# Optimization experiments

Hardware: AMD Instinct MI355X
Metric: run time of the kernel (lower is better)

Reference implementation:

```python
import jax, jax.numpy as jnp
import numpy as np

B = 4096
P_HID = 1024
H_HID = 512
MAX_P = 128
MAX_HE = MAX_P // 3  # 42
TAU = 1.0
EPS = 1e-20


def setup_inputs() -> dict:
    key = jax.random.key(0)
    ks = jax.random.split(key, 12)
    s_p = 1.0 / np.sqrt(P_HID)
    s_h = 1.0 / np.sqrt(H_HID)
    # gumbel noise: g = -log(-log(U))
    u_p = jax.random.uniform(ks[3], (B, MAX_P, 2), minval=EPS, maxval=1.0)
    u_h = jax.random.uniform(ks[4], (B, MAX_HE, 2), minval=EPS, maxval=1.0)
    return {
        "particle_h": jax.random.normal(ks[0], (B, P_HID), jnp.float32),
        "edge_h": jax.random.normal(ks[1], (B, H_HID), jnp.float32),
        "hyperedge_h": jax.random.normal(ks[2], (B, H_HID), jnp.float32),
        "g_p": -jnp.log(-jnp.log(u_p)),
        "g_h": -jnp.log(-jnp.log(u_h)),
        "W1_p": jax.random.normal(ks[5], (P_HID, P_HID), jnp.float32) * s_p,
        "b1_p": jnp.zeros((P_HID,), jnp.float32),
        "W2_p": jax.random.normal(ks[6], (P_HID, MAX_P), jnp.float32) * s_p,
        "b2_p": jnp.zeros((MAX_P,), jnp.float32),
        "W1_h": jax.random.normal(ks[7], (H_HID, H_HID), jnp.float32) * s_h,
        "b1_h": jnp.zeros((H_HID,), jnp.float32),
        "W2_h": jax.random.normal(ks[8], (H_HID, MAX_HE), jnp.float32) * s_h,
        "b2_h": jnp.zeros((MAX_HE,), jnp.float32),
    }


def _gumbel_hard_st(logits, g, tau):
    """F.gumbel_softmax(stack([l,-l],-1), tau, hard=True)[...,0] (straight-through)."""
    y = jax.nn.softmax((jnp.stack([logits, -logits], axis=-1) + g) / tau, axis=-1)
    y0 = y[..., 0]
    hard0 = (y0 > y[..., 1]).astype(y0.dtype)
    return hard0 + y0 - jax.lax.stop_gradient(y0)


def _mlp(x, W1, b1, W2, b2):
    return jax.nn.gelu(x @ W1 + b1, approximate=False) @ W2 + b2


def reference(particle_h, edge_h, hyperedge_h, g_p, g_h,
              W1_p, b1_p, W2_p, b2_p, W1_h, b1_h, W2_h, b2_h):
    particle_logits = _mlp(particle_h, W1_p, b1_p, W2_p, b2_p)      # [B, MAX_P]
    particle_mask = _gumbel_hard_st(particle_logits, g_p, TAU)      # [B, MAX_P]
    n_particles = particle_mask.sum(axis=-1).astype(jnp.int32)      # [B]

    # Ragged edge lists as a fixed padded buffer: all C(MAX_P,2) lexicographic
    # pairs (same order as torch.combinations); pair (i,j), i<j, is valid for
    # batch b iff j < n_particles[b].
    ii, jj = jnp.triu_indices(MAX_P, k=1)
    edge_index = jnp.stack([ii, jj]).astype(jnp.int32)              # [2, E_max]
    edge_valid = jj[None, :] < n_particles[:, None]                 # [B, E_max] bool

    hyperedge_logits = _mlp(hyperedge_h, W1_h, b1_h, W2_h, b2_h)    # [B, MAX_HE]
    hyperedge_mask = _gumbel_hard_st(hyperedge_logits, g_h, TAU)
    n_hyperedges = hyperedge_mask.sum(axis=-1).astype(jnp.int32)

    return (particle_mask, n_particles, edge_index, edge_valid,
            hyperedge_mask, n_hyperedges)
```

## Files before the change

### kernel.cpp

```cpp
#include <hip/hip_runtime.h>
#include <hip/hip_bf16.h>
#include <math.h>

typedef __bf16 bf16_t;
typedef bf16_t bf16x8 __attribute__((ext_vector_type(8)));
typedef bf16_t bf16x4 __attribute__((ext_vector_type(4)));
typedef float f32x4 __attribute__((ext_vector_type(4)));
typedef int i32x4 __attribute__((ext_vector_type(4)));
typedef unsigned int u32;

#define B_SZ 4096
#define P_HID 1024
#define H_HID 512
#define MAX_P 128
#define MAX_HE 42
#define HE_PAD 128
#define E_MAX 8128
#define E_MAX4 2032

__device__ __forceinline__ void async_cp16(const bf16_t* g, bf16_t* l) {
    __builtin_amdgcn_global_load_lds(
        (const __attribute__((address_space(1))) u32*)g,
        (__attribute__((address_space(3))) u32*)l, 16, 0, 0);
}

__device__ __forceinline__ float gelu_exact(float v) {
    return 0.5f * v * (1.f + erff(v * 0.70710678118654752f));
}

struct GemmP {
    const bf16_t *Ahi, *Alo, *BThi, *BTlo;
    const float* bias;
    bf16_t *Chi, *Clo;
    const float* g;
    float *out_mask, *out_n;
    int *ws_n;
    int N, K, NV, nx;
};

template<int MODE, int BM>
__global__ __launch_bounds__(256, 3) void gemm_pack(GemmP P, GemmP H, int pBlocks)
{
    constexpr int BN = 128;
    constexpr int MT = BM / 32;
    constexpr int NT = 4;
    constexpr int OPS_A = BM / 16;
    constexpr int OPS_B = BN / 16;
    constexpr int NOPS = 2 * OPS_A + 2 * OPS_B;
    constexpr int TILE = NOPS * 16 * 32;

    __shared__ __align__(16) bf16_t smem[2 * TILE];
    __shared__ float cnt[BM][2];

    const bool isP = (int)blockIdx.x < pBlocks;
    const GemmP& a = isP ? P : H;
    const int bid  = isP ? blockIdx.x : blockIdx.x - pBlocks;
    const int bn   = (bid % a.nx) * BN;
    const int bm   = (bid / a.nx) * BM;
    const int K    = a.K;

    const int tid  = threadIdx.x;
    const int lane = tid & 63;
    const int wid  = tid >> 6;
    const int wm   = wid & 1;
    const int wn   = wid >> 1;

    const int srow = lane >> 2;
    const int scol = (lane & 3) * 8;
    const int fr   = lane & 15;
    const int fq   = lane >> 4;

    f32x4 acc[MT][NT];
#pragma unroll
    for (int i = 0; i < MT; ++i)
#pragma unroll
        for (int j = 0; j < NT; ++j)
            acc[i][j] = (f32x4){0.f, 0.f, 0.f, 0.f};

    const bf16_t* const gA0 = a.Ahi  + (size_t)bm * K;
    const bf16_t* const gA1 = a.Alo  + (size_t)bm * K;
    const bf16_t* const gB0 = a.BThi + (size_t)bn * K;
    const bf16_t* const gB1 = a.BTlo + (size_t)bn * K;

    auto stage = [&](int buf, int kt) {
#pragma unroll
        for (int o = 0; o < NOPS; ++o) {
            if ((o & 3) != wid) continue;
            const bf16_t* gsrc;
            int q, sec;
            if (o < OPS_A)                  { q = o;                     gsrc = gA0; sec = 0; }
            else if (o < 2 * OPS_A)         { q = o - OPS_A;             gsrc = gA1; sec = BM * 32; }
            else if (o < 2 * OPS_A + OPS_B) { q = o - 2 * OPS_A;         gsrc = gB0; sec = 2 * BM * 32; }
            else                            { q = o - 2 * OPS_A - OPS_B; gsrc = gB1; sec = 2 * BM * 32 + BN * 32; }
            async_cp16(gsrc + (size_t)(q * 16 + srow) * K + kt + scol,
                       smem + buf * TILE + sec + q * 16 * 32);
        }
    };

    stage(0, 0);
    __syncthreads();
    int cur = 0;
    for (int kt = 0; kt < K; kt += 32) {
        if (kt + 32 < K) stage(cur ^ 1, kt + 32);

        const bf16_t* const Tb = smem + cur * TILE;
        bf16x8 ah[MT], al[MT];
#pragma unroll
        for (int i = 0; i < MT; ++i) {
            const int row = wm * (BM / 2) + i * 16 + fr;
            ah[i] = *(const bf16x8*)(Tb + row * 32 + fq * 8);
            al[i] = *(const bf16x8*)(Tb + BM * 32 + row * 32 + fq * 8);
        }
#pragma unroll
        for (int j = 0; j < NT; ++j) {
            const int row = wn * 64 + j * 16 + fr;
            const bf16x8 bh = *(const bf16x8*)(Tb + 2 * BM * 32 + row * 32 + fq * 8);
            const bf16x8 bl = *(const bf16x8*)(Tb + 2 * BM * 32 + BN * 32 + row * 32 + fq * 8);
#pragma unroll
            for (int i = 0; i < MT; ++i) {
                acc[i][j] = __builtin_amdgcn_mfma_f32_16x16x32_bf16(ah[i], bh, acc[i][j], 0, 0, 0);
                acc[i][j] = __builtin_amdgcn_mfma_f32_16x16x32_bf16(ah[i], bl, acc[i][j], 0, 0, 0);
                acc[i][j] = __builtin_amdgcn_mfma_f32_16x16x32_bf16(al[i], bh, acc[i][j], 0, 0, 0);
            }
        }
        __syncthreads();
        cur ^= 1;
    }

    if (MODE == 0) {
#pragma unroll
        for (int i = 0; i < MT; ++i)
#pragma unroll
            for (int j = 0; j < NT; ++j) {
                const int col  = bn + wn * 64 + j * 16 + fr;
                const int row0 = bm + wm * (BM / 2) + i * 16 + fq * 4;
                const float bj = a.bias[col];
#pragma unroll
                for (int r = 0; r < 4; ++r) {
                    float v = gelu_exact(acc[i][j][r] + bj);
                    bf16_t h = (bf16_t)v;
                    bf16_t l = (bf16_t)(v - (float)h);
                    const size_t off = (size_t)(row0 + r) * a.N + col;
                    a.Chi[off] = h;
                    a.Clo[off] = l;
                }
            }
    } else {
        const int NV = a.NV;
#pragma unroll
        for (int i = 0; i < MT; ++i) {
#pragma unroll
            for (int r = 0; r < 4; ++r) {
                const int row_l = wm * (BM / 2) + i * 16 + fq * 4 + r;
                const int grow  = bm + row_l;
                float s = 0.f;
#pragma unroll
                for (int j = 0; j < NT; ++j) {
                    const int col = wn * 64 + j * 16 + fr;
                    if (col < NV) {
                        const float v = acc[i][j][r] + a.bias[col];
                        const size_t idx = (size_t)grow * NV + col;
                        const float g0 = a.g[2 * idx + 0];
                        const float g1 = a.g[2 * idx + 1];
                        const float m = ((v + g0) > (g1 - v)) ? 1.f : 0.f;
                        a.out_mask[idx] = m;
                        s += m;
                    }
                }
                s += __shfl_xor(s, 1, 64);
                s += __shfl_xor(s, 2, 64);
                s += __shfl_xor(s, 4, 64);
                s += __shfl_xor(s, 8, 64);
                if (fr == 0) cnt[row_l][wn] = s;
            }
        }
        __syncthreads();
        if (tid < BM) {
            const float c = cnt[tid][0] + cnt[tid][1];
            a.out_n[bm + tid] = c;
            if (a.ws_n) a.ws_n[bm + tid] = (int)c;
        }
    }
}

struct PrepArgs {
    const float *ph, *hh, *W1p, *W2p, *W1h, *W2h;
    bf16_t *pA_hi, *pA_lo, *hA_hi, *hA_lo;
    bf16_t *W1pT_hi, *W1pT_lo, *W2pT_hi, *W2pT_lo;
    bf16_t *W1hT_hi, *W1hT_lo, *W2hT_hi, *W2hT_lo;
    float *out_ei; int *ws_jj;
};

__device__ __forceinline__ void split4(const float* x, bf16_t* hi, bf16_t* lo, int i) {
    float4 v = ((const float4*)x)[i];
    float vv[4] = {v.x, v.y, v.z, v.w};
    bf16x4 h, l;
#pragma unroll
    for (int r = 0; r < 4; ++r) {
        bf16_t hh = (bf16_t)vv[r];
        h[r] = hh;
        l[r] = (bf16_t)(vv[r] - (float)hh);
    }
    ((bf16x4*)hi)[i] = h;
    ((bf16x4*)lo)[i] = l;
}

__device__ __forceinline__ void tsplit(
    const float* W, bf16_t* Thi, bf16_t* Tlo, int K, int N,
    int t, int nx, float (*sh)[33], int tid)
{
    const int n0 = (t % nx) * 32, k0 = (t / nx) * 32;
    const int tx = tid & 31, ty = tid >> 5;
    for (int r = ty; r < 32; r += 8) {
        const int n = n0 + tx;
        sh[r][tx] = (n < N) ? W[(size_t)(k0 + r) * N + n] : 0.f;
    }
    __syncthreads();
    for (int r = ty; r < 32; r += 8) {
        const float x = sh[tx][r];
        bf16_t h = (bf16_t)x;
        bf16_t l = (bf16_t)(x - (float)h);
        const size_t off = (size_t)(n0 + r) * K + k0 + tx;
        Thi[off] = h;
        Tlo[off] = l;
    }
}

__device__ __forceinline__ int tri_off(int i) { return (i * (255 - i)) >> 1; }

__global__ __launch_bounds__(256) void prep_all(PrepArgs a)
{
    __shared__ float sh[32][33];
    const int bid = blockIdx.x;
    const int tid = threadIdx.x;

    if (bid < 4096) {
        split4(a.ph, a.pA_hi, a.pA_lo, bid * 256 + tid);
    } else if (bid < 6144) {
        split4(a.hh, a.hA_hi, a.hA_lo, (bid - 4096) * 256 + tid);
    } else if (bid < 7168) {
        tsplit(a.W1p, a.W1pT_hi, a.W1pT_lo, P_HID, P_HID, bid - 6144, 32, sh, tid);
    } else if (bid < 7296) {
        tsplit(a.W2p, a.W2pT_hi, a.W2pT_lo, P_HID, MAX_P, bid - 7168, 4, sh, tid);
    } else if (bid < 7552) {
        tsplit(a.W1h, a.W1hT_hi, a.W1hT_lo, H_HID, H_HID, bid - 7296, 16, sh, tid);
    } else if (bid < 7616) {
        tsplit(a.W2h, a.W2hT_hi, a.W2hT_lo, H_HID, MAX_HE, bid - 7552, 4, sh, tid);
    } else {
        const int e = (bid - 7616) * 256 + tid;
        if (e < E_MAX) {
            int i = (int)((255.0 - sqrt(65025.0 - 8.0 * (double)e)) * 0.5);
            if (i < 0) i = 0;
            if (i > 126) i = 126;
            while (i > 0 && tri_off(i) > e) --i;
            while (i < 126 && tri_off(i + 1) <= e) ++i;
            const int j = i + 1 + (e - tri_off(i));
            a.out_ei[e] = (float)i;
            a.out_ei[E_MAX + e] = (float)j;
            a.ws_jj[e] = j;
        }
    }
}

__global__ __launch_bounds__(256) void edge_valid_kernel(
    const int* __restrict__ ws_jj, const int* __restrict__ ws_n,
    float* __restrict__ out)
{
    const int b   = blockIdx.x >> 1;
    const int seg = blockIdx.x & 1;
    const int n   = ws_n[b];
    const int base = seg * (E_MAX4 / 2);
    float* const orow = out + (size_t)b * E_MAX;
#pragma unroll
    for (int it = 0; it < 4; ++it) {
        const int q = base + it * 256 + threadIdx.x;
        if (q < base + E_MAX4 / 2) {
            const i32x4 j4 = ((const i32x4*)ws_jj)[q];
            f32x4 v;
            v.x = (j4.x < n) ? 1.f : 0.f;
            v.y = (j4.y < n) ? 1.f : 0.f;
            v.z = (j4.z < n) ? 1.f : 0.f;
            v.w = (j4.w < n) ? 1.f : 0.f;
            __builtin_nontemporal_store(v, &((f32x4*)orow)[q]);
        }
    }
}

extern "C" void kernel_launch(void* const* d_in, const int* in_sizes, int n_in,
                              void* d_out, int out_size, void* d_ws, size_t ws_size,
                              hipStream_t stream)
{
    const float* particle_h  = (const float*)d_in[0];
    const float* hyperedge_h = (const float*)d_in[2];
    const float* g_p  = (const float*)d_in[3];
    const float* g_h  = (const float*)d_in[4];
    const float* W1_p = (const float*)d_in[5];
    const float* b1_p = (const float*)d_in[6];
    const float* W2_p = (const float*)d_in[7];
    const float* b2_p = (const float*)d_in[8];
    const float* W1_h = (const float*)d_in[9];
    const float* b1_h = (const float*)d_in[10];
    const float* W2_h = (const float*)d_in[11];
    const float* b2_h = (const float*)d_in[12];

    float* out = (float*)d_out;
    float* out_pmask = out;
    float* out_np    = out_pmask + (size_t)B_SZ * MAX_P;
    float* out_ei    = out_np + B_SZ;
    float* out_ev    = out_ei + 2 * E_MAX;
    float* out_hmask = out_ev + (size_t)B_SZ * E_MAX;
    float* out_nh    = out_hmask + (size_t)B_SZ * MAX_HE;

    char* w = (char*)d_ws;
    bf16_t* pA_hi   = (bf16_t*)w;  w += (size_t)B_SZ * P_HID * 2;
    bf16_t* pA_lo   = (bf16_t*)w;  w += (size_t)B_SZ * P_HID * 2;
    bf16_t* hA_hi   = (bf16_t*)w;  w += (size_t)B_SZ * H_HID * 2;
    bf16_t* hA_lo   = (bf16_t*)w;  w += (size_t)B_SZ * H_HID * 2;
    bf16_t* hidp_hi = (bf16_t*)w;  w += (size_t)B_SZ * P_HID * 2;
    bf16_t* hidp_lo = (bf16_t*)w;  w += (size_t)B_SZ * P_HID * 2;
    bf16_t* hidh_hi = (bf16_t*)w;  w += (size_t)B_SZ * H_HID * 2;
    bf16_t* hidh_lo = (bf16_t*)w;  w += (size_t)B_SZ * H_HID * 2;
    bf16_t* W1pT_hi = (bf16_t*)w;  w += (size_t)P_HID * P_HID * 2;
    bf16_t* W1pT_lo = (bf16_t*)w;  w += (size_t)P_HID * P_HID * 2;
    bf16_t* W2pT_hi = (bf16_t*)w;  w += (size_t)MAX_P * P_HID * 2;
    bf16_t* W2pT_lo = (bf16_t*)w;  w += (size_t)MAX_P * P_HID * 2;
    bf16_t* W1hT_hi = (bf16_t*)w;  w += (size_t)H_HID * H_HID * 2;
    bf16_t* W1hT_lo = (bf16_t*)w;  w += (size_t)H_HID * H_HID * 2;
    bf16_t* W2hT_hi = (bf16_t*)w;  w += (size_t)HE_PAD * H_HID * 2;
    bf16_t* W2hT_lo = (bf16_t*)w;  w += (size_t)HE_PAD * H_HID * 2;
    int*    ws_np   = (int*)w;     w += B_SZ * 4;
    int*    ws_jj   = (int*)w;

    PrepArgs pa;
    pa.ph = particle_h; pa.hh = hyperedge_h;
    pa.W1p = W1_p; pa.W2p = W2_p; pa.W1h = W1_h; pa.W2h = W2_h;
    pa.pA_hi = pA_hi; pa.pA_lo = pA_lo; pa.hA_hi = hA_hi; pa.hA_lo = hA_lo;
    pa.W1pT_hi = W1pT_hi; pa.W1pT_lo = W1pT_lo;
    pa.W2pT_hi = W2pT_hi; pa.W2pT_lo = W2pT_lo;
    pa.W1hT_hi = W1hT_hi; pa.W1hT_lo = W1hT_lo;
    pa.W2hT_hi = W2hT_hi; pa.W2hT_lo = W2hT_lo;
    pa.out_ei = out_ei; pa.ws_jj = ws_jj;
    prep_all<<<7648, 256, 0, stream>>>(pa);

    {
        GemmP P = {}, H = {};
        P.Ahi = pA_hi;  P.Alo = pA_lo;  P.BThi = W1pT_hi; P.BTlo = W1pT_lo;
        P.bias = b1_p;  P.Chi = hidp_hi; P.Clo = hidp_lo;
        P.N = P_HID; P.K = P_HID; P.nx = P_HID / 128;
        H.Ahi = hA_hi;  H.Alo = hA_lo;  H.BThi = W1hT_hi; H.BTlo = W1hT_lo;
        H.bias = b1_h;  H.Chi = hidh_hi; H.Clo = hidh_lo;
        H.N = H_HID; H.K = H_HID; H.nx = H_HID / 128;
        const int pB = (B_SZ / 64) * P.nx;
        const int hB = (B_SZ / 64) * H.nx;
        gemm_pack<0, 64><<<pB + hB, 256, 0, stream>>>(P, H, pB);
    }

    {
        GemmP P = {}, H = {};
        P.Ahi = hidp_hi; P.Alo = hidp_lo; P.BThi = W2pT_hi; P.BTlo = W2pT_lo;
        P.bias = b2_p; P.g = g_p; P.out_mask = out_pmask; P.out_n = out_np;
        P.ws_n = ws_np; P.N = MAX_P; P.K = P_HID; P.NV = MAX_P; P.nx = 1;
        H.Ahi = hidh_hi; H.Alo = hidh_lo; H.BThi = W2hT_hi; H.BTlo = W2hT_lo;
        H.bias = b2_h; H.g = g_h; H.out_mask = out_hmask; H.out_n = out_nh;
        H.ws_n = nullptr; H.N = HE_PAD; H.K = H_HID; H.NV = MAX_HE; H.nx = 1;
        const int pB = B_SZ / 32;
        const int hB = B_SZ / 32;
        gemm_pack<1, 32><<<pB + hB, 256, 0, stream>>>(P, H, pB);
    }

    edge_valid_kernel<<<2 * B_SZ, 256, 0, stream>>>(ws_jj, ws_np, out_ev);
}
```

Measured before the change: 274.4 us.

## Split-K the second-layer logit GEMM with atomic-counter last-block reduction

Replaces the second-layer GEMM launch (256 blocks of 32 rows) with a split-K kernel that divides K into 4 slices, so 1024 blocks run. Each block writes fp32 partial tiles into scratch memory reused from the dead pA_hi buffer. An atomic per-tile counter picks the last block to sum the partials, add bias, apply the Gumbel comparison and write masks and counts. This targets low occupancy on the small-N GEMM, at the cost of partial-sum traffic, fences and an extra counter reset in the prep kernel.

```diff
diff --git a/kernel.cpp b/kernel.cpp
--- a/kernel.cpp
+++ b/kernel.cpp
@@ -183,12 +183,154 @@
     }
 }
 
+struct GemmSK {
+    const bf16_t *Ahi, *Alo, *BThi, *BTlo;
+    const float* bias;
+    const float* g;
+    float *out_mask, *out_n;
+    int *ws_n;
+    float* part;
+    int* cnt;
+    int K, NV;
+};
+
+__global__ __launch_bounds__(256, 4) void gemm_logit_sk(GemmSK P, GemmSK H, int pBlocks)
+{
+    constexpr int SPLITS = 4;
+    constexpr int BM = 32, BN = 128, NT = 4;
+    constexpr int OPS_A = BM / 16;
+    constexpr int OPS_B = BN / 16;
+    constexpr int NOPS  = 2 * OPS_A + 2 * OPS_B;
+    constexpr int TILE  = NOPS * 16 * 32;
+
+    __shared__ __align__(16) bf16_t smem[2 * TILE];
+
+    const bool isP = (int)blockIdx.x < pBlocks;
+    const GemmSK& a = isP ? P : H;
+    const int bid   = isP ? blockIdx.x : blockIdx.x - pBlocks;
+    const int tile  = bid >> 2;
+    const int split = bid & (SPLITS - 1);
+    const int bm    = tile * BM;
+    const int K     = a.K;
+    const int Ksub  = K / SPLITS;
+    const int k0    = split * Ksub;
+
+    const int tid  = threadIdx.x;
+    const int lane = tid & 63;
+    const int wid  = tid >> 6;
+    const int wm   = wid & 1;
+    const int wn   = wid >> 1;
+
+    const int srow = lane >> 2;
+    const int scol = (lane & 3) * 8;
+    const int fr   = lane & 15;
+    const int fq   = lane >> 4;
+
+    f32x4 acc[NT];
+#pragma unroll
+    for (int j = 0; j < NT; ++j) acc[j] = (f32x4){0.f, 0.f, 0.f, 0.f};
+
+    const bf16_t* const gA0 = a.Ahi  + (size_t)bm * K + k0;
+    const bf16_t* const gA1 = a.Alo  + (size_t)bm * K + k0;
+    const bf16_t* const gB0 = a.BThi + k0;
+    const bf16_t* const gB1 = a.BTlo + k0;
+
+    auto stage = [&](int buf, int kt) {
+#pragma unroll
+        for (int o = 0; o < NOPS; ++o) {
+            if ((o & 3) != wid) continue;
+            const bf16_t* gsrc;
+            int q, sec;
+            if (o < OPS_A)                  { q = o;                     gsrc = gA0; sec = 0; }
+            else if (o < 2 * OPS_A)         { q = o - OPS_A;             gsrc = gA1; sec = BM * 32; }
+            else if (o < 2 * OPS_A + OPS_B) { q = o - 2 * OPS_A;         gsrc = gB0; sec = 2 * BM * 32; }
+            else                            { q = o - 2 * OPS_A - OPS_B; gsrc = gB1; sec = 2 * BM * 32 + BN * 32; }
+            async_cp16(gsrc + (size_t)(q * 16 + srow) * K + kt + scol,
+                       smem + buf * TILE + sec + q * 16 * 32);
+        }
+    };
+
+    stage(0, 0);
+    __syncthreads();
+    int cur = 0;
+    for (int kt = 0; kt < Ksub; kt += 32) {
+        if (kt + 32 < Ksub) stage(cur ^ 1, kt + 32);
+
+        const bf16_t* const Tb = smem + cur * TILE;
+        const int arow = wm * 16 + fr;
+        const bf16x8 ah = *(const bf16x8*)(Tb + arow * 32 + fq * 8);
+        const bf16x8 al = *(const bf16x8*)(Tb + BM * 32 + arow * 32 + fq * 8);
+#pragma unroll
+        for (int j = 0; j < NT; ++j) {
+            const int brow = wn * 64 + j * 16 + fr;
+            const bf16x8 bh = *(const bf16x8*)(Tb + 2 * BM * 32 + brow * 32 + fq * 8);
+            const bf16x8 bl = *(const bf16x8*)(Tb + 2 * BM * 32 + BN * 32 + brow * 32 + fq * 8);
+            acc[j] = __builtin_amdgcn_mfma_f32_16x16x32_bf16(ah, bh, acc[j], 0, 0, 0);
+            acc[j] = __builtin_amdgcn_mfma_f32_16x16x32_bf16(ah, bl, acc[j], 0, 0, 0);
+            acc[j] = __builtin_amdgcn_mfma_f32_16x16x32_bf16(al, bh, acc[j], 0, 0, 0);
+        }
+        __syncthreads();
+        cur ^= 1;
+    }
+
+    float* const pt = a.part + ((size_t)tile * SPLITS + split) * (BM * BN);
+#pragma unroll
+    for (int j = 0; j < NT; ++j)
+#pragma unroll
+        for (int r = 0; r < 4; ++r) {
+            const int row_l = wm * 16 + fq * 4 + r;
+            const int col   = wn * 64 + j * 16 + fr;
+            pt[row_l * BN + col] = acc[j][r];
+        }
+    __threadfence();
+    __syncthreads();
+
+    int* const sflag = (int*)smem;
+    if (tid == 0) {
+        const int old = atomicAdd(a.cnt + tile, 1);
+        *sflag = (old == SPLITS - 1) ? 1 : 0;
+    }
+    __syncthreads();
+    if (*sflag == 0) return;
+    __threadfence();
+
+    const float* const base = a.part + (size_t)tile * SPLITS * (BM * BN);
+    const int row   = tid >> 3;
+    const int grow  = bm + row;
+    const int cbase = tid & 7;
+    const int NV    = a.NV;
+    float s = 0.f;
+#pragma unroll
+    for (int c = 0; c < 16; ++c) {
+        const int col = cbase + c * 8;
+        float v = a.bias[col];
+#pragma unroll
+        for (int sp = 0; sp < SPLITS; ++sp)
+            v += base[sp * (BM * BN) + row * BN + col];
+        if (col < NV) {
+            const size_t idx = (size_t)grow * NV + col;
+            const float g0 = a.g[2 * idx + 0];
+            const float g1 = a.g[2 * idx + 1];
+            const float m = ((v + g0) > (g1 - v)) ? 1.f : 0.f;
+            a.out_mask[idx] = m;
+            s += m;
+        }
+    }
+    s += __shfl_xor(s, 1, 64);
+    s += __shfl_xor(s, 2, 64);
+    s += __shfl_xor(s, 4, 64);
+    if ((tid & 7) == 0) {
+        a.out_n[grow] = s;
+        if (a.ws_n) a.ws_n[grow] = (int)s;
+    }
+}
+
 struct PrepArgs {
     const float *ph, *hh, *W1p, *W2p, *W1h, *W2h;
     bf16_t *pA_hi, *pA_lo, *hA_hi, *hA_lo;
     bf16_t *W1pT_hi, *W1pT_lo, *W2pT_hi, *W2pT_lo;
     bf16_t *W1hT_hi, *W1hT_lo, *W2hT_hi, *W2hT_lo;
-    float *out_ei; int *ws_jj;
+    float *out_ei; int *ws_jj; int *ws_cnt;
 };
 
 __device__ __forceinline__ void split4(const float* x, bf16_t* hi, bf16_t* lo, int i) {
@@ -246,7 +388,7 @@
         tsplit(a.W1h, a.W1hT_hi, a.W1hT_lo, H_HID, H_HID, bid - 7296, 16, sh, tid);
     } else if (bid < 7616) {
         tsplit(a.W2h, a.W2hT_hi, a.W2hT_lo, H_HID, MAX_HE, bid - 7552, 4, sh, tid);
-    } else {
+    } else if (bid < 7648) {
         const int e = (bid - 7616) * 256 + tid;
         if (e < E_MAX) {
             int i = (int)((255.0 - sqrt(65025.0 - 8.0 * (double)e)) * 0.5);
@@ -259,6 +401,8 @@
             a.out_ei[E_MAX + e] = (float)j;
             a.ws_jj[e] = j;
         }
+    } else {
+        a.ws_cnt[tid] = 0;
     }
 }
 
@@ -329,7 +473,10 @@
     bf16_t* W2hT_hi = (bf16_t*)w;  w += (size_t)HE_PAD * H_HID * 2;
     bf16_t* W2hT_lo = (bf16_t*)w;  w += (size_t)HE_PAD * H_HID * 2;
     int*    ws_np   = (int*)w;     w += B_SZ * 4;
-    int*    ws_jj   = (int*)w;
+    int*    ws_jj   = (int*)w;     w += E_MAX * 4;
+    int*    ws_cnt  = (int*)w;     w += 256 * 4;
+
+    float* part_base = (float*)pA_hi;
 
     PrepArgs pa;
     pa.ph = particle_h; pa.hh = hyperedge_h;
@@ -339,8 +486,8 @@
     pa.W2pT_hi = W2pT_hi; pa.W2pT_lo = W2pT_lo;
     pa.W1hT_hi = W1hT_hi; pa.W1hT_lo = W1hT_lo;
     pa.W2hT_hi = W2hT_hi; pa.W2hT_lo = W2hT_lo;
-    pa.out_ei = out_ei; pa.ws_jj = ws_jj;
-    prep_all<<<7648, 256, 0, stream>>>(pa);
+    pa.out_ei = out_ei; pa.ws_jj = ws_jj; pa.ws_cnt = ws_cnt;
+    prep_all<<<7649, 256, 0, stream>>>(pa);
 
     {
         GemmP P = {}, H = {};
@@ -356,16 +503,18 @@
     }
 
     {
-        GemmP P = {}, H = {};
+        GemmSK P = {}, H = {};
         P.Ahi = hidp_hi; P.Alo = hidp_lo; P.BThi = W2pT_hi; P.BTlo = W2pT_lo;
         P.bias = b2_p; P.g = g_p; P.out_mask = out_pmask; P.out_n = out_np;
-        P.ws_n = ws_np; P.N = MAX_P; P.K = P_HID; P.NV = MAX_P; P.nx = 1;
+        P.ws_n = ws_np; P.part = part_base; P.cnt = ws_cnt;
+        P.K = P_HID; P.NV = MAX_P;
         H.Ahi = hidh_hi; H.Alo = hidh_lo; H.BThi = W2hT_hi; H.BTlo = W2hT_lo;
         H.bias = b2_h; H.g = g_h; H.out_mask = out_hmask; H.out_n = out_nh;
-        H.ws_n = nullptr; H.N = HE_PAD; H.K = H_HID; H.NV = MAX_HE; H.nx = 1;
-        const int pB = B_SZ / 32;
-        const int hB = B_SZ / 32;
-        gemm_pack<1, 32><<<pB + hB, 256, 0, stream>>>(P, H, pB);
+        H.ws_n = nullptr; H.part = part_base + (size_t)128 * 4 * 32 * 128;
+        H.cnt = ws_cnt + 128; H.K = H_HID; H.NV = MAX_HE;
+        const int pB = (B_SZ / 32) * 4;
+        const int hB = (B_SZ / 32) * 4;
+        gemm_logit_sk<<<pB + hB, 256, 0, stream>>>(P, H, pB);
     }
 
     edge_valid_kernel<<<2 * B_SZ, 256, 0, stream>>>(ws_jj, ws_np, out_ev);
```

Result: slower. 452.1 us (+64.8%).
